# Kernel tuning notes

Measured on AMD Instinct MI355X. Metric: run time of the kernel, lower is better.

Reference implementation:

```python
import jax, jax.numpy as jnp
import numpy as np

NUM_CLASSES = 80
IMG_SIZE = 640.0
STRIDE = 8.0
NUM_ANCHORS = 3
EPS = 1e-7


def setup_inputs() -> dict:
    key = jax.random.key(0)
    k1, k2, k3, k4 = jax.random.split(key, 4)
    B, N, S = 16, 32, 80
    preds = jax.random.normal(k1, (B, NUM_ANCHORS * (5 + NUM_CLASSES), S, S), dtype=jnp.float32)
    targets_cls = jax.random.randint(k2, (B, N), 0, NUM_CLASSES)
    xy = jax.random.uniform(k3, (B, N, 2), dtype=jnp.float32)                       # normalized centers in [0,1)
    wh = jax.random.uniform(k4, (B, N, 2), dtype=jnp.float32, minval=0.02, maxval=0.5)  # normalized w,h
    targets_box = jnp.concatenate([xy, wh], axis=-1)
    anchors = jnp.array([[10.0, 13.0], [16.0, 30.0], [33.0, 23.0]], dtype=jnp.float32)
    return {"preds": preds, "anchors": anchors, "targets_cls": targets_cls, "targets_box": targets_box}


def _bce_logits(logits, targets):
    # BCEWithLogits: softplus(l) - l*t (stable)
    return jax.nn.softplus(logits) - logits * targets


def _masked_mean(x, mask):
    m = mask.astype(x.dtype)
    return jnp.sum(x * m) / jnp.maximum(jnp.sum(m), 1.0)


def _ciou(pb, tb):
    px1, py1, px2, py2 = pb[..., 0], pb[..., 1], pb[..., 2], pb[..., 3]
    tx1, ty1, tx2, ty2 = tb[..., 0], tb[..., 1], tb[..., 2], tb[..., 3]
    iw = jnp.maximum(jnp.minimum(px2, tx2) - jnp.maximum(px1, tx1), 0.0)
    ih = jnp.maximum(jnp.minimum(py2, ty2) - jnp.maximum(py1, ty1), 0.0)
    inter = iw * ih
    pa = jnp.maximum(px2 - px1, 0.0) * jnp.maximum(py2 - py1, 0.0)
    ta = jnp.maximum(tx2 - tx1, 0.0) * jnp.maximum(ty2 - ty1, 0.0)
    union = pa + ta - inter + EPS
    iou = inter / union
    center_dist = ((px1 + px2) / 2 - (tx1 + tx2) / 2) ** 2 + ((py1 + py2) / 2 - (ty1 + ty2) / 2) ** 2
    enc_diag = (jnp.maximum(px2, tx2) - jnp.minimum(px1, tx1)) ** 2 + (jnp.maximum(py2, ty2) - jnp.minimum(py1, ty1)) ** 2 + EPS
    pw = jnp.maximum(px2 - px1, EPS)
    ph = jnp.maximum(py2 - py1, EPS)
    tw = jnp.maximum(tx2 - tx1, EPS)
    th = jnp.maximum(ty2 - ty1, EPS)
    v = (4.0 / np.pi ** 2) * (jnp.arctan(tw / th) - jnp.arctan(pw / ph)) ** 2
    alpha = jax.lax.stop_gradient(v / (1.0 - iou + v + EPS))  # torch.no_grad() in original
    return iou - center_dist / enc_diag - alpha * v


def _yolo_loss(preds, anchors, targets_cls, targets_box):
    B, _, S, _ = preds.shape
    A, C = NUM_ANCHORS, NUM_CLASSES
    p = preds.reshape(B, A, 5 + C, S, S).transpose(0, 1, 3, 4, 2)  # [B,A,S,S,5+C]

    # ---- vectorized target -> anchor matching (replaces python loops) ----
    x, y, w, h = targets_box[..., 0], targets_box[..., 1], targets_box[..., 2], targets_box[..., 3]
    gx, gy = x * S, y * S
    gi = jnp.clip(jnp.floor(gx), 0, S - 1).astype(jnp.int32)  # [B,N]
    gj = jnp.clip(jnp.floor(gy), 0, S - 1).astype(jnp.int32)
    tw_px, th_px = w * IMG_SIZE, h * IMG_SIZE
    aw, ah = anchors[:, 0], anchors[:, 1]
    # IoU of (0,0,w,h) target vs (0,0,aw,ah) anchors: inter = min(w,aw)*min(h,ah)
    inter = jnp.minimum(tw_px[..., None], aw) * jnp.minimum(th_px[..., None], ah)  # [B,N,A]
    union = tw_px[..., None] * th_px[..., None] + aw * ah - inter
    best_a = jnp.argmax(inter / union, axis=-1).astype(jnp.int32)  # [B,N]

    N = targets_box.shape[1]
    bf = jnp.broadcast_to(jnp.arange(B)[:, None], (B, N)).reshape(-1)
    af = best_a.reshape(-1)
    gjf = gj.reshape(-1)
    gif = gi.reshape(-1)

    obj = jnp.zeros((B, A, S, S), dtype=bool).at[bf, af, gjf, gif].set(True)
    tcls = jnp.zeros((B, A, S, S, C), dtype=preds.dtype).at[bf, af, gjf, gif, targets_cls.reshape(-1)].set(1.0)
    cx, cy = x * IMG_SIZE, y * IMG_SIZE
    tboxes = jnp.stack([cx - tw_px / 2, cy - th_px / 2, cx + tw_px / 2, cy + th_px / 2], axis=-1).reshape(-1, 4)
    tgt_xyxy = jnp.zeros((B, A, S, S, 4), dtype=preds.dtype).at[bf, af, gjf, gif].set(tboxes)

    # ---- decode predictions ----
    grid = jnp.arange(S, dtype=preds.dtype)
    pcx = (jax.nn.sigmoid(p[..., 0]) + grid[None, None, None, :]) * STRIDE  # grid_x varies along last axis
    pcy = (jax.nn.sigmoid(p[..., 1]) + grid[None, None, :, None]) * STRIDE  # grid_y varies along row axis
    pw = aw.reshape(1, A, 1, 1) * jnp.exp(p[..., 2])
    ph = ah.reshape(1, A, 1, 1) * jnp.exp(p[..., 3])
    pred_xyxy = jnp.stack([pcx - pw / 2, pcy - ph / 2, pcx + pw / 2, pcy + ph / 2], axis=-1)

    # ---- losses (masked means instead of boolean gathers, same math) ----
    ciou = _ciou(pred_xyxy, tgt_xyxy)
    loss_ciou = 1.0 - _masked_mean(ciou, obj)
    pred_conf = p[..., 4]
    loss_conf_obj = _masked_mean(_bce_logits(pred_conf, 1.0), obj)
    loss_conf_noobj = _masked_mean(_bce_logits(pred_conf, 0.0), jnp.logical_not(obj))
    cls_mask = jnp.broadcast_to(obj[..., None], tcls.shape)
    loss_cls = _masked_mean(_bce_logits(p[..., 5:], tcls), cls_mask)
    return loss_ciou + loss_conf_obj + 0.5 * loss_conf_noobj + loss_cls


def reference(preds, anchors, targets_cls, targets_box):
    return _yolo_loss(preds, anchors, targets_cls, targets_box)
```

## Files before the change

kernel.cpp:

```cpp
#include <hip/hip_runtime.h>
#include <math.h>

constexpr int B = 16, A = 3, S = 80, C = 80, N = 32;
constexpr int CELLS = B * A * S * S;
constexpr int CH = 5 + C;
constexpr int PLANE = S * S;
constexpr float EPS = 1e-7f;

constexpr int N_DENSE_BLK = 300;
constexpr size_t OBJ_OFF = 4096;
constexpr int NT = B * N;

__device__ __forceinline__ float softplusf(float x) {
    return fmaxf(x, 0.0f) + log1pf(expf(-fabsf(x)));
}

__device__ __forceinline__ void cell_of(const float* __restrict__ tbox,
                                        const float* aw, const float* ah,
                                        int idx, int& gi, int& gj, int& ba) {
    float x = tbox[idx * 4 + 0], y = tbox[idx * 4 + 1];
    float w = tbox[idx * 4 + 2], h = tbox[idx * 4 + 3];
    gi = min(max((int)floorf(x * (float)S), 0), S - 1);
    gj = min(max((int)floorf(y * (float)S), 0), S - 1);
    float tw = w * 640.0f, th = h * 640.0f;
    ba = 0; float best = -1.0f;
    #pragma unroll
    for (int a = 0; a < A; a++) {
        float inter = fminf(tw, aw[a]) * fminf(th, ah[a]);
        float uni = tw * th + aw[a] * ah[a] - inter;
        float r = inter / uni;
        if (r > best) { best = r; ba = a; }
    }
}

__global__ void __launch_bounds__(256) yolo_dense(const float* __restrict__ preds,
                                                  double* __restrict__ densePart) {
    int g = blockIdx.x * 256 + threadIdx.x;
    int p = g / 1600;
    int r = g - p * 1600;
    int b = p / 3, a = p - b * 3;
    const float4* src = (const float4*)preds;
    float4 v = src[(size_t)(b * (A * CH) + a * CH + 4) * (PLANE / 4) + r];
    float s = softplusf(v.x) + softplusf(v.y) + softplusf(v.z) + softplusf(v.w);
    #pragma unroll
    for (int off = 32; off > 0; off >>= 1) s += __shfl_down(s, off);
    __shared__ float sm[4];
    int wave = threadIdx.x >> 6, lane = threadIdx.x & 63;
    if (lane == 0) sm[wave] = s;
    __syncthreads();
    if (threadIdx.x == 0)
        densePart[blockIdx.x] = (double)(sm[0] + sm[1] + sm[2] + sm[3]);
}

__global__ void __launch_bounds__(256) yolo_obj(const float* __restrict__ preds,
                                                const float* __restrict__ anchors,
                                                const int* __restrict__ tcls,
                                                const float* __restrict__ tbox,
                                                float* __restrict__ objPart) {
    int wave = threadIdx.x >> 6, lane = threadIdx.x & 63;
    int t = blockIdx.x * 4 + wave;
    int b = t >> 5, n = t & 31;

    float aw[A], ah[A];
    #pragma unroll
    for (int a = 0; a < A; a++) { aw[a] = anchors[a * 2]; ah[a] = anchors[a * 2 + 1]; }

    int gi, gj, ba;
    cell_of(tbox, aw, ah, b * N + n, gi, gj, ba);

    bool winner = true;
    for (int n2 = n + 1; n2 < N; n2++) {
        int gi2, gj2, ba2;
        cell_of(tbox, aw, ah, b * N + n2, gi2, gj2, ba2);
        if (gi2 == gi && gj2 == gj && ba2 == ba) { winner = false; break; }
    }

    float r_ciou = 0.f, r_obj = 0.f, r_corr = 0.f, r_cls = 0.f, r_cnt = 0.f;
    if (winner) {
        int base = (b * (A * CH) + ba * CH) * PLANE + gj * S + gi;
        int cls = tcls[b * N + n];
        float l0 = preds[base + (5 + lane) * PLANE];
        float scls = softplusf(l0) - ((lane == cls) ? l0 : 0.f);
        if (lane < C - 64) {
            float l1 = preds[base + (5 + 64 + lane) * PLANE];
            scls += softplusf(l1) - (((64 + lane) == cls) ? l1 : 0.f);
        }
        #pragma unroll
        for (int off = 32; off > 0; off >>= 1) scls += __shfl_down(scls, off);
        r_cls = scls;

        float conf = preds[base + 4 * PLANE];
        float sp = softplusf(conf);
        r_obj = sp - conf;
        r_corr = sp;
        r_cnt = 1.f;
        float tx = preds[base + 0 * PLANE], ty = preds[base + 1 * PLANE];
        float twl = preds[base + 2 * PLANE], thl = preds[base + 3 * PLANE];
        float pcx = (1.0f / (1.0f + expf(-tx)) + (float)gi) * 8.0f;
        float pcy = (1.0f / (1.0f + expf(-ty)) + (float)gj) * 8.0f;
        float pw = aw[ba] * expf(twl), ph = ah[ba] * expf(thl);
        float px1 = pcx - pw * 0.5f, px2 = pcx + pw * 0.5f;
        float py1 = pcy - ph * 0.5f, py2 = pcy + ph * 0.5f;
        int ti = (b * N + n) * 4;
        float cx = tbox[ti + 0] * 640.0f, cy = tbox[ti + 1] * 640.0f;
        float tw = tbox[ti + 2] * 640.0f, th = tbox[ti + 3] * 640.0f;
        float tx1 = cx - tw * 0.5f, tx2 = cx + tw * 0.5f;
        float ty1 = cy - th * 0.5f, ty2 = cy + th * 0.5f;
        float iw = fmaxf(fminf(px2, tx2) - fmaxf(px1, tx1), 0.0f);
        float ih = fmaxf(fminf(py2, ty2) - fmaxf(py1, ty1), 0.0f);
        float inter = iw * ih;
        float pa = fmaxf(px2 - px1, 0.0f) * fmaxf(py2 - py1, 0.0f);
        float ta = fmaxf(tx2 - tx1, 0.0f) * fmaxf(ty2 - ty1, 0.0f);
        float uni = pa + ta - inter + EPS;
        float iou = inter / uni;
        float dx = (px1 + px2) * 0.5f - (tx1 + tx2) * 0.5f;
        float dy = (py1 + py2) * 0.5f - (ty1 + ty2) * 0.5f;
        float cdist = dx * dx + dy * dy;
        float ew = fmaxf(px2, tx2) - fminf(px1, tx1);
        float eh = fmaxf(py2, ty2) - fminf(py1, ty1);
        float ediag = ew * ew + eh * eh + EPS;
        float pwc = fmaxf(px2 - px1, EPS), phc = fmaxf(py2 - py1, EPS);
        float twc = fmaxf(tx2 - tx1, EPS), thc = fmaxf(ty2 - ty1, EPS);
        float dv = atanf(twc / thc) - atanf(pwc / phc);
        float v = (float)(4.0 / (M_PI * M_PI)) * dv * dv;
        float alpha = v / (1.0f - iou + v + EPS);
        r_ciou = iou - cdist / ediag - alpha * v;
    }
    if (lane == 0) {
        float* dst = objPart + (size_t)t * 8;
        dst[0] = r_ciou; dst[1] = r_obj; dst[2] = r_corr; dst[3] = r_cls; dst[4] = r_cnt;
    }
}

__global__ void __launch_bounds__(256) yolo_fin(const double* __restrict__ densePart,
                                                const float* __restrict__ objPart,
                                                float* __restrict__ out) {
    double sp = 0, ciou = 0, obj = 0, corr = 0, cls = 0, cnt = 0;
    for (int i = threadIdx.x; i < N_DENSE_BLK; i += 256) sp += densePart[i];
    for (int t = threadIdx.x; t < NT; t += 256) {
        const float* p = objPart + (size_t)t * 8;
        ciou += p[0]; obj += p[1]; corr += p[2]; cls += p[3]; cnt += p[4];
    }
    #pragma unroll
    for (int off = 32; off > 0; off >>= 1) {
        sp   += __shfl_down(sp, off);   ciou += __shfl_down(ciou, off);
        obj  += __shfl_down(obj, off);  corr += __shfl_down(corr, off);
        cls  += __shfl_down(cls, off);  cnt  += __shfl_down(cnt, off);
    }
    __shared__ double sm[6][4];
    int wave = threadIdx.x >> 6, lane = threadIdx.x & 63;
    if (lane == 0) {
        sm[0][wave] = sp;  sm[1][wave] = ciou; sm[2][wave] = obj;
        sm[3][wave] = corr; sm[4][wave] = cls; sm[5][wave] = cnt;
    }
    __syncthreads();
    if (threadIdx.x == 0) {
        double T[6];
        for (int k = 0; k < 6; k++) T[k] = sm[k][0] + sm[k][1] + sm[k][2] + sm[k][3];
        double nobj = T[5];
        double noobj_sum = T[0] - T[3];
        double d_obj = fmax(nobj, 1.0);
        double d_no  = fmax((double)CELLS - nobj, 1.0);
        double d_cls = fmax(nobj * (double)C, 1.0);
        double loss = (1.0 - T[1] / d_obj) + T[2] / d_obj
                    + 0.5 * (noobj_sum / d_no) + T[4] / d_cls;
        out[0] = (float)loss;
    }
}

extern "C" void kernel_launch(void* const* d_in, const int* in_sizes, int n_in,
                              void* d_out, int out_size, void* d_ws, size_t ws_size,
                              hipStream_t stream) {
    const float* preds   = (const float*)d_in[0];
    const float* anchors = (const float*)d_in[1];
    const int*   tcls    = (const int*)d_in[2];
    const float* tbox    = (const float*)d_in[3];

    double* densePart = (double*)d_ws;
    float*  objPart   = (float*)((char*)d_ws + OBJ_OFF);

    yolo_dense<<<N_DENSE_BLK, 256, 0, stream>>>(preds, densePart);
    yolo_obj<<<NT / 4, 256, 0, stream>>>(preds, anchors, tcls, tbox, objPart);
    yolo_fin<<<1, 256, 0, stream>>>(densePart, objPart, (float*)d_out);
}
```

Before: 148.9 us.

## Fuse dense and object kernels into one launch with ballot-based duplicate detection

Merges the dense softplus-reduction kernel and the per-target object kernel into a single launch, with block index selecting the role. This removes one kernel launch and lets both parts run concurrently. The per-target serial scan over later targets, which found duplicate cell assignments, is replaced by each lane computing one target's cell key followed by a wave shuffle and ballot. The per-target partial results are also written as float4 stores. Correctness depends on the ballot mask covering lanes above n within the first 32 lanes.

Measured after the change: 140.3 us. 5.8% less time.

```diff
diff --git a/kernel.cpp b/kernel.cpp
--- a/kernel.cpp
+++ b/kernel.cpp
@@ -8,76 +8,74 @@
 constexpr float EPS = 1e-7f;
 
 constexpr int N_DENSE_BLK = 300;
+constexpr int NT = B * N;
+constexpr int N_OBJ_BLK = NT / 4;
 constexpr size_t OBJ_OFF = 4096;
-constexpr int NT = B * N;
 
 __device__ __forceinline__ float softplusf(float x) {
     return fmaxf(x, 0.0f) + log1pf(expf(-fabsf(x)));
 }
 
-__device__ __forceinline__ void cell_of(const float* __restrict__ tbox,
-                                        const float* aw, const float* ah,
-                                        int idx, int& gi, int& gj, int& ba) {
-    float x = tbox[idx * 4 + 0], y = tbox[idx * 4 + 1];
-    float w = tbox[idx * 4 + 2], h = tbox[idx * 4 + 3];
-    gi = min(max((int)floorf(x * (float)S), 0), S - 1);
-    gj = min(max((int)floorf(y * (float)S), 0), S - 1);
-    float tw = w * 640.0f, th = h * 640.0f;
-    ba = 0; float best = -1.0f;
-    #pragma unroll
-    for (int a = 0; a < A; a++) {
-        float inter = fminf(tw, aw[a]) * fminf(th, ah[a]);
-        float uni = tw * th + aw[a] * ah[a] - inter;
-        float r = inter / uni;
-        if (r > best) { best = r; ba = a; }
+__global__ void __launch_bounds__(256) yolo_fused(const float* __restrict__ preds,
+                                                  const float* __restrict__ anchors,
+                                                  const int* __restrict__ tcls,
+                                                  const float* __restrict__ tbox,
+                                                  double* __restrict__ densePart,
+                                                  float* __restrict__ objPart) {
+    int wave = threadIdx.x >> 6, lane = threadIdx.x & 63;
+
+    if (blockIdx.x < N_DENSE_BLK) {
+        int g = blockIdx.x * 256 + threadIdx.x;
+        int p = g / 1600;
+        int r = g - p * 1600;
+        int b = p / 3, a = p - b * 3;
+        const float4* src = (const float4*)preds;
+        float4 v = src[(size_t)(b * (A * CH) + a * CH + 4) * (PLANE / 4) + r];
+        float s = softplusf(v.x) + softplusf(v.y) + softplusf(v.z) + softplusf(v.w);
+        #pragma unroll
+        for (int off = 32; off > 0; off >>= 1) s += __shfl_down(s, off);
+        __shared__ float sm[4];
+        if (lane == 0) sm[wave] = s;
+        __syncthreads();
+        if (threadIdx.x == 0)
+            densePart[blockIdx.x] = (double)(sm[0] + sm[1] + sm[2] + sm[3]);
+        return;
     }
-}
 
-__global__ void __launch_bounds__(256) yolo_dense(const float* __restrict__ preds,
-                                                  double* __restrict__ densePart) {
-    int g = blockIdx.x * 256 + threadIdx.x;
-    int p = g / 1600;
-    int r = g - p * 1600;
-    int b = p / 3, a = p - b * 3;
-    const float4* src = (const float4*)preds;
-    float4 v = src[(size_t)(b * (A * CH) + a * CH + 4) * (PLANE / 4) + r];
-    float s = softplusf(v.x) + softplusf(v.y) + softplusf(v.z) + softplusf(v.w);
-    #pragma unroll
-    for (int off = 32; off > 0; off >>= 1) s += __shfl_down(s, off);
-    __shared__ float sm[4];
-    int wave = threadIdx.x >> 6, lane = threadIdx.x & 63;
-    if (lane == 0) sm[wave] = s;
-    __syncthreads();
-    if (threadIdx.x == 0)
-        densePart[blockIdx.x] = (double)(sm[0] + sm[1] + sm[2] + sm[3]);
-}
-
-__global__ void __launch_bounds__(256) yolo_obj(const float* __restrict__ preds,
-                                                const float* __restrict__ anchors,
-                                                const int* __restrict__ tcls,
-                                                const float* __restrict__ tbox,
-                                                float* __restrict__ objPart) {
-    int wave = threadIdx.x >> 6, lane = threadIdx.x & 63;
-    int t = blockIdx.x * 4 + wave;
+    int t = (blockIdx.x - N_DENSE_BLK) * 4 + wave;
     int b = t >> 5, n = t & 31;
 
     float aw[A], ah[A];
     #pragma unroll
     for (int a = 0; a < A; a++) { aw[a] = anchors[a * 2]; ah[a] = anchors[a * 2 + 1]; }
 
-    int gi, gj, ba;
-    cell_of(tbox, aw, ah, b * N + n, gi, gj, ba);
-
-    bool winner = true;
-    for (int n2 = n + 1; n2 < N; n2++) {
-        int gi2, gj2, ba2;
-        cell_of(tbox, aw, ah, b * N + n2, gi2, gj2, ba2);
-        if (gi2 == gi && gj2 == gj && ba2 == ba) { winner = false; break; }
+    int key = -1;
+    if (lane < N) {
+        float4 tb = ((const float4*)tbox)[b * N + lane];
+        int gi = min(max((int)floorf(tb.x * (float)S), 0), S - 1);
+        int gj = min(max((int)floorf(tb.y * (float)S), 0), S - 1);
+        float tw = tb.z * 640.0f, th = tb.w * 640.0f;
+        int ba = 0; float best = -1.0f;
+        #pragma unroll
+        for (int a = 0; a < A; a++) {
+            float inter = fminf(tw, aw[a]) * fminf(th, ah[a]);
+            float uni = tw * th + aw[a] * ah[a] - inter;
+            float r = inter / uni;
+            if (r > best) { best = r; ba = a; }
+        }
+        key = (ba * S + gj) * S + gi;
     }
+    int my_key = __shfl(key, n);
+    unsigned long long eq = __ballot(key == my_key);
+    bool winner = (eq & 0xFFFFFFFFull & ~((2ull << n) - 1ull)) == 0;
 
     float r_ciou = 0.f, r_obj = 0.f, r_corr = 0.f, r_cls = 0.f, r_cnt = 0.f;
     if (winner) {
+        int ba = my_key / (S * S);
+        int rem = my_key - ba * (S * S);
+        int gj = rem / S, gi = rem - gj * S;
         int base = (b * (A * CH) + ba * CH) * PLANE + gj * S + gi;
+
         int cls = tcls[b * N + n];
         float l0 = preds[base + (5 + lane) * PLANE];
         float scls = softplusf(l0) - ((lane == cls) ? l0 : 0.f);
@@ -128,7 +126,8 @@
     }
     if (lane == 0) {
         float* dst = objPart + (size_t)t * 8;
-        dst[0] = r_ciou; dst[1] = r_obj; dst[2] = r_corr; dst[3] = r_cls; dst[4] = r_cnt;
+        ((float4*)dst)[0] = make_float4(r_ciou, r_obj, r_corr, r_cls);
+        ((float4*)dst)[1] = make_float4(r_cnt, 0.f, 0.f, 0.f);
     }
 }
 
@@ -179,7 +178,7 @@
     double* densePart = (double*)d_ws;
     float*  objPart   = (float*)((char*)d_ws + OBJ_OFF);
 
-    yolo_dense<<<N_DENSE_BLK, 256, 0, stream>>>(preds, densePart);
-    yolo_obj<<<NT / 4, 256, 0, stream>>>(preds, anchors, tcls, tbox, objPart);
+    yolo_fused<<<N_DENSE_BLK + N_OBJ_BLK, 256, 0, stream>>>(
+        preds, anchors, tcls, tbox, densePart, objPart);
     yolo_fin<<<1, 256, 0, stream>>>(densePart, objPart, (float*)d_out);
 }
```
